# Optimization experiments

Hardware: AMD Instinct MI355X
Metric: run time of the kernel (lower is better)

Reference implementation:

```python
import jax, jax.numpy as jnp
import numpy as np

G, N, E, F, D = 4096, 64, 256, 64, 128
H1, H2 = 16, 2
EP = 32768
EPS = 1e-15
MAX_LOGSTD = 10.0


def setup_inputs() -> dict:
    key = jax.random.key(0)
    ks = jax.random.split(key, 16)
    def lin(k, i, o):
        return (jax.random.normal(k, (i, o), jnp.float32) / np.sqrt(i)).astype(jnp.float32)
    inp = {}
    inp["x"] = jax.random.normal(ks[0], (G, N, F), jnp.float32)
    inp["edge_index"] = jax.random.randint(ks[1], (G, 2, E), 0, N, dtype=jnp.int32)
    inp["edge_weight"] = jax.random.uniform(ks[2], (G, E), jnp.float32)
    inp["pos_edges"] = jax.random.randint(ks[3], (2, EP), 0, G, dtype=jnp.int32)
    inp["neg_edges"] = jax.random.randint(ks[4], (2, EP), 0, G, dtype=jnp.int32)
    inp["eps"] = jax.random.normal(ks[5], (G, D), jnp.float32)
    inp["W_gcn1"] = lin(ks[6], F, D); inp["b_gcn1"] = jnp.zeros((D,), jnp.float32)
    inp["W_fc1"] = lin(ks[7], D, H1); inp["b_fc1"] = jnp.zeros((H1,), jnp.float32)
    inp["W_fc2"] = lin(ks[8], H1, H2); inp["b_fc2"] = jnp.zeros((H2,), jnp.float32)
    inp["W_c1"] = lin(ks[9], D, 2 * D); inp["b_c1"] = jnp.zeros((2 * D,), jnp.float32)
    inp["W_mu"] = lin(ks[10], 2 * D, D); inp["b_mu"] = jnp.zeros((D,), jnp.float32)
    inp["W_ls"] = lin(ks[11], 2 * D, D); inp["b_ls"] = jnp.zeros((D,), jnp.float32)
    inp["emb"] = jax.random.normal(ks[12], (G, D), jnp.float32)
    inp["W_lin1"] = lin(ks[13], 2 * D, 2 * D); inp["b_lin1"] = jnp.zeros((2 * D,), jnp.float32)
    inp["W_lin2"] = lin(ks[14], 2 * D, 2 * D); inp["b_lin2"] = jnp.zeros((2 * D,), jnp.float32)
    return inp


def gcn_conv(x, src, dst, w, W, b, n):
    # PyG GCNConv: add self-loops (weight 1), sym-normalize, aggregate at target (col).
    xw = x @ W                                      # [n, out]
    deg = jnp.zeros((n,), xw.dtype).at[dst].add(w) + 1.0
    dinv = jax.lax.rsqrt(deg)
    norm = dinv[src] * w * dinv[dst]
    agg = jnp.zeros_like(xw).at[dst].add(xw[src] * norm[:, None])
    agg = agg + xw * (dinv * dinv)[:, None]         # self-loop term
    return agg + b


def sage_graph(x, ei, w, W_gcn1, b_gcn1, W_fc1, b_fc1, W_fc2, b_fc2):
    src, dst = ei[0], ei[1]
    h = gcn_conv(x, src, dst, w, W_gcn1, b_gcn1, N)          # [N, D]
    a1 = jnp.tanh(h @ W_fc1 + b_fc1)                         # [N, H1]
    S = jax.nn.softmax(a1 @ W_fc2 + b_fc2, axis=1)           # [N, 2]
    # get_laplacian(normalization='sym'): L = I - D^{-1/2} A D^{-1/2}, deg from row
    deg = jnp.zeros((N,), x.dtype).at[src].add(w)
    dinv = jnp.where(deg > 0, jax.lax.rsqrt(jnp.maximum(deg, 1e-30)), 0.0)
    lw = -dinv[src] * w * dinv[dst]
    L = jnp.zeros((N, N), x.dtype).at[src, dst].add(lw) + jnp.eye(N, dtype=x.dtype)
    new_adj = S.T @ (L @ S)                                  # [2, 2]
    norm_adj = new_adj / jnp.maximum(jnp.sum(jnp.abs(new_adj), axis=1, keepdims=True), 1e-12)
    diag = jnp.diagonal(norm_adj)
    pos_penalty = jnp.mean((diag - 1.0) ** 2)                # MSE vs ones(2)
    g_emb = jnp.mean(S.T @ h, axis=0)                        # [D]
    return g_emb, pos_penalty


def gcn_conv_unw(x, src, dst, W, b, n):
    return gcn_conv(x, src, dst, jnp.ones(src.shape, x.dtype), W, b, n)


def reference(x, edge_index, edge_weight, pos_edges, neg_edges, eps,
              W_gcn1, b_gcn1, W_fc1, b_fc1, W_fc2, b_fc2,
              W_c1, b_c1, W_mu, b_mu, W_ls, b_ls, emb,
              W_lin1, b_lin1, W_lin2, b_lin2):
    g_embs, pens = jax.vmap(sage_graph,
                            in_axes=(0, 0, 0, None, None, None, None, None, None))(
        x, edge_index, edge_weight, W_gcn1, b_gcn1, W_fc1, b_fc1, W_fc2, b_fc2)
    positive_penalty = jnp.mean(pens)
    # VGAE encode over graph-level graph (dropout in eval mode = identity)
    ps, pd = pos_edges[0], pos_edges[1]
    h = jax.nn.relu(gcn_conv_unw(g_embs, ps, pd, W_c1, b_c1, G))
    mu = gcn_conv_unw(h, ps, pd, W_mu, b_mu, G)
    logstd = jnp.minimum(gcn_conv_unw(h, ps, pd, W_ls, b_ls, G), MAX_LOGSTD)
    z = mu + eps * jnp.exp(logstd)                            # reparametrize
    zc = jnp.concatenate([emb, z], axis=-1)                   # [G, 2D]
    def pred(ei):
        fx = zc[ei[0]] @ W_lin1 + b_lin1
        fy = zc[ei[1]] @ W_lin2 + b_lin2
        return jax.nn.sigmoid(jnp.sum(fx * fy, axis=1))
    pos_pred = pred(pos_edges)
    neg_pred = pred(neg_edges)
    rec_loss = -jnp.mean(jnp.log(pos_pred + EPS)) - jnp.mean(jnp.log(1.0 - neg_pred + EPS))
    kl = -0.5 * jnp.mean(jnp.sum(1.0 + 2.0 * logstd - mu ** 2 - jnp.exp(2.0 * logstd), axis=1))
    pre_loss = rec_loss + kl / G
    return pre_loss, positive_penalty, pos_pred, neg_pred
```

## Files before the change

kernel.cpp:

```cpp
#include <hip/hip_runtime.h>
#include <hip/hip_bf16.h>
#include <math.h>

#define GG   4096
#define NNODE 64
#define EEDGE 256
#define FFEAT 64
#define DDIM 128
#define EP   32768

__global__ void k_prep(const float* __restrict__ Wg, const float* __restrict__ Wf1,
                       const float* __restrict__ bf1, const float* __restrict__ bg,
                       float* __restrict__ Wgf1, float* __restrict__ bcomb,
                       float* __restrict__ bg32) {
    int t = threadIdx.x;
    for (int o = t; o < 1024; o += 256) {
        int f = o >> 4, j = o & 15;
        float s = 0.f;
        for (int d = 0; d < 128; ++d) s += Wg[f * 128 + d] * Wf1[d * 16 + j];
        Wgf1[o] = s;
    }
    if (t < 16) {
        float s = bf1[t];
        for (int d = 0; d < 128; ++d) s += bg[d] * Wf1[d * 16 + t];
        bcomb[t] = s;
    }
    if (t >= 128) bg32[t - 128] = 32.0f * bg[t - 128];
}

__global__ __launch_bounds__(256) void k_pg(
    const float* __restrict__ x, const int* __restrict__ ei, const float* __restrict__ ew,
    const float* __restrict__ Wgf1, const float* __restrict__ bcomb,
    const float* __restrict__ Wf2, const float* __restrict__ bf2,
    float* __restrict__ Qh, float* __restrict__ pens)
{
    __shared__ __align__(16) float sm[8464];
    float* xs    = sm;
    float* Wgf1s = sm + 4352;
    float* a1s   = sm + 5376;
    int*   srcs  = (int*)(sm + 6400);
    int*   dsts  = (int*)(sm + 6656);
    float* lwx   = sm + 6912;
    int*   lsrc  = (int*)(sm + 7168);
    float* lnrm  = sm + 7424;
    int*   icnt  = (int*)(sm + 7680);
    int*   offs  = (int*)(sm + 7744);
    int*   curs  = (int*)(sm + 7808);
    float* degw  = sm + 7872;
    float* dinvs = sm + 7936;
    float* deg2s = sm + 8000;
    float* dinv2s= sm + 8064;
    float* Ss    = sm + 8128;
    float* Ssum  = sm + 8256;
    float* LSs   = sm + 8320;
    float* bcs   = sm + 8448;

    const int g = blockIdx.x;
    const int t = threadIdx.x;
    const float* xg = x + (size_t)g * 4096;

    {
        const int* eg = ei + (size_t)g * 512;
        srcs[t] = eg[t];
        dsts[t] = eg[256 + t];
        lwx[t]  = ew[(size_t)g * 256 + t];
        for (int i = t; i < 1024; i += 256) {
            int n = i >> 4, k = (i & 15) * 4;
            *(float4*)&xs[n * 68 + k] = *(const float4*)&xg[n * 64 + k];
        }
        for (int i = t; i < 1024; i += 256) Wgf1s[i] = Wgf1[i];
        if (t < 16) bcs[t] = bcomb[t];
        if (t < 64) { icnt[t] = 0; degw[t] = 1.0f; deg2s[t] = 0.0f; }
        if (t < 128) LSs[t] = 0.0f;
    }
    __syncthreads();

    {
        int dd = dsts[t], s = srcs[t];
        float w = lwx[t];
        atomicAdd(&icnt[dd], 1);
        atomicAdd(&degw[dd], w);
        atomicAdd(&deg2s[s], w);
    }
    __syncthreads();

    if (t < 64) {
        int v = icnt[t], own = v;
        for (int o = 1; o < 64; o <<= 1) { int u = __shfl_up(v, o); if (t >= o) v += u; }
        int excl = v - own;
        offs[t] = excl; curs[t] = excl;
        dinvs[t] = rsqrtf(degw[t]);
        float dg = deg2s[t];
        dinv2s[t] = dg > 0.0f ? rsqrtf(fmaxf(dg, 1e-30f)) : 0.0f;
    }
    __syncthreads();

    {
        int s = srcs[t], dd = dsts[t];
        float w = lwx[t];
        int pos = atomicAdd(&curs[dd], 1);
        lsrc[pos] = s;
        lnrm[pos] = dinvs[s] * w * dinvs[dd];
        lwx[t] = -dinv2s[s] * w * dinv2s[dd];
    }
    __syncthreads();

    {
        int n = t >> 2, base = (t & 3) * 16;
        float sc = dinvs[n] * dinvs[n];
        const float* xrow = &xs[n * 68 + base];
        float4 A0 = *(const float4*)&xrow[0];
        float4 A1 = *(const float4*)&xrow[4];
        float4 A2 = *(const float4*)&xrow[8];
        float4 A3 = *(const float4*)&xrow[12];
        A0.x *= sc; A0.y *= sc; A0.z *= sc; A0.w *= sc;
        A1.x *= sc; A1.y *= sc; A1.z *= sc; A1.w *= sc;
        A2.x *= sc; A2.y *= sc; A2.z *= sc; A2.w *= sc;
        A3.x *= sc; A3.y *= sc; A3.z *= sc; A3.w *= sc;
        int o = offs[n], c = icnt[n];
        for (int j = 0; j < c; ++j) {
            int s = lsrc[o + j];
            float nm = lnrm[o + j];
            const float* xr = &xs[s * 68 + base];
            float4 X0 = *(const float4*)&xr[0];
            float4 X1 = *(const float4*)&xr[4];
            float4 X2 = *(const float4*)&xr[8];
            float4 X3 = *(const float4*)&xr[12];
            A0.x += X0.x * nm; A0.y += X0.y * nm; A0.z += X0.z * nm; A0.w += X0.w * nm;
            A1.x += X1.x * nm; A1.y += X1.y * nm; A1.z += X1.z * nm; A1.w += X1.w * nm;
            A2.x += X2.x * nm; A2.y += X2.y * nm; A2.z += X2.z * nm; A2.w += X2.w * nm;
            A3.x += X3.x * nm; A3.y += X3.y * nm; A3.z += X3.z * nm; A3.w += X3.w * nm;
        }
        __syncthreads();
        float* xw = &xs[n * 68 + base];
        *(float4*)&xw[0]  = A0;
        *(float4*)&xw[4]  = A1;
        *(float4*)&xw[8]  = A2;
        *(float4*)&xw[12] = A3;
    }
    __syncthreads();

    {
        int n = t >> 2, j0 = (t & 3) * 4;
        float a0 = bcs[j0], a1v = bcs[j0 + 1], a2 = bcs[j0 + 2], a3 = bcs[j0 + 3];
#pragma unroll 4
        for (int k4 = 0; k4 < 16; ++k4) {
            float4 hv = *(const float4*)&xs[n * 68 + k4 * 4];
            float4 w0 = *(const float4*)&Wgf1s[(k4 * 4 + 0) * 16 + j0];
            float4 w1 = *(const float4*)&Wgf1s[(k4 * 4 + 1) * 16 + j0];
            float4 w2 = *(const float4*)&Wgf1s[(k4 * 4 + 2) * 16 + j0];
            float4 w3 = *(const float4*)&Wgf1s[(k4 * 4 + 3) * 16 + j0];
            a0  += hv.x * w0.x + hv.y * w1.x + hv.z * w2.x + hv.w * w3.x;
            a1v += hv.x * w0.y + hv.y * w1.y + hv.z * w2.y + hv.w * w3.y;
            a2  += hv.x * w0.z + hv.y * w1.z + hv.z * w2.z + hv.w * w3.z;
            a3  += hv.x * w0.w + hv.y * w1.w + hv.z * w2.w + hv.w * w3.w;
        }
        a1s[n * 16 + j0]     = tanhf(a0);
        a1s[n * 16 + j0 + 1] = tanhf(a1v);
        a1s[n * 16 + j0 + 2] = tanhf(a2);
        a1s[n * 16 + j0 + 3] = tanhf(a3);
    }
    __syncthreads();

    if (t < 128) {
        int n = t >> 1, kk = t & 1;
        float z = bf2[kk];
#pragma unroll
        for (int j = 0; j < 16; ++j) z += a1s[n * 16 + j] * Wf2[j * 2 + kk];
        Ss[n * 2 + kk] = z;
    }
    __syncthreads();

    if (t < 64) {
        float z0 = Ss[t * 2], z1 = Ss[t * 2 + 1];
        float m = fmaxf(z0, z1);
        float e0 = expf(z0 - m), e1 = expf(z1 - m);
        float inv = 1.0f / (e0 + e1);
        e0 *= inv; e1 *= inv;
        Ss[t * 2] = e0; Ss[t * 2 + 1] = e1;
        Ssum[t] = e0 + e1;
    }
    __syncthreads();

    for (int i = t; i < 512; i += 256) {
        int e = i >> 1, kk = i & 1;
        atomicAdd(&LSs[srcs[e] * 2 + kk], lwx[e] * Ss[dsts[e] * 2 + kk]);
    }
    __syncthreads();

    if (t < 64) {
        float s0 = Ss[t * 2], s1 = Ss[t * 2 + 1];
        float l0 = s0 + LSs[t * 2], l1 = s1 + LSs[t * 2 + 1];
        float p00 = s0 * l0, p01 = s0 * l1, p10 = s1 * l0, p11 = s1 * l1;
        for (int o = 32; o; o >>= 1) {
            p00 += __shfl_down(p00, o); p01 += __shfl_down(p01, o);
            p10 += __shfl_down(p10, o); p11 += __shfl_down(p11, o);
        }
        if (t == 0) {
            float r0 = fmaxf(fabsf(p00) + fabsf(p01), 1e-12f);
            float r1 = fmaxf(fabsf(p10) + fabsf(p11), 1e-12f);
            float d0 = p00 / r0 - 1.0f, d1 = p11 / r1 - 1.0f;
            pens[g] = 0.5f * (d0 * d0 + d1 * d1);
        }
    }
    {
        int k = t & 63, p = t >> 6;
        float qk = 0.f;
#pragma unroll 4
        for (int n = p * 16; n < p * 16 + 16; ++n)
            qk += Ssum[n] * xs[n * 68 + k];
        __syncthreads();
        a1s[p * 64 + k] = qk;
    }
    __syncthreads();
    if (t < 64)
        Qh[(size_t)g * 64 + t] = 0.5f * (a1s[t] + a1s[64 + t] + a1s[128 + t] + a1s[192 + t]);
}

__global__ void k_cnt(const int* __restrict__ pd, int* __restrict__ icnt) {
    int e = blockIdx.x * 256 + threadIdx.x;
    atomicAdd(&icnt[pd[e]], 1);
}

__global__ void k_scan(const int* __restrict__ icnt, int* __restrict__ offs,
                       int* __restrict__ curs, float* __restrict__ dinv) {
    __shared__ int wsum[4];
    int t = threadIdx.x;
    int base = t * 16;
    int l0,l1,l2,l3,l4,l5,l6,l7,l8,l9,l10,l11,l12,l13,l14,l15;
    l0=icnt[base+0]; l1=icnt[base+1]; l2=icnt[base+2]; l3=icnt[base+3];
    l4=icnt[base+4]; l5=icnt[base+5]; l6=icnt[base+6]; l7=icnt[base+7];
    l8=icnt[base+8]; l9=icnt[base+9]; l10=icnt[base+10]; l11=icnt[base+11];
    l12=icnt[base+12]; l13=icnt[base+13]; l14=icnt[base+14]; l15=icnt[base+15];
    int s = l0+l1+l2+l3+l4+l5+l6+l7+l8+l9+l10+l11+l12+l13+l14+l15;
    int lane = t & 63, w = t >> 6;
    int v = s;
    for (int o = 1; o < 64; o <<= 1) { int u = __shfl_up(v, o); if (lane >= o) v += u; }
    if (lane == 63) wsum[w] = v;
    __syncthreads();
    int woff = 0;
    for (int i = 0; i < 4; ++i) if (i < w) woff += wsum[i];
    int run = woff + v - s;
#define SC(L, I) offs[base+(I)] = run; curs[base+(I)] = run; \
    dinv[base+(I)] = rsqrtf((float)(L) + 1.0f); run += L;
    SC(l0,0) SC(l1,1) SC(l2,2) SC(l3,3) SC(l4,4) SC(l5,5) SC(l6,6) SC(l7,7)
    SC(l8,8) SC(l9,9) SC(l10,10) SC(l11,11) SC(l12,12) SC(l13,13) SC(l14,14) SC(l15,15)
#undef SC
}

__global__ void k_place(const int* __restrict__ pe, const float* __restrict__ dinv,
                        int* __restrict__ curs, int* __restrict__ csr_src,
                        float* __restrict__ csr_nrm) {
    int e = blockIdx.x * 256 + threadIdx.x;
    int s = pe[e], d = pe[EP + e];
    int pos = atomicAdd(&curs[d], 1);
    csr_src[pos] = s;
    csr_nrm[pos] = dinv[s] * dinv[d];
}

__global__ void k_gather128(const int* __restrict__ offs, const int* __restrict__ icnt,
                            const int* __restrict__ csr_src, const float* __restrict__ csr_nrm,
                            const float* __restrict__ dinv, const float* __restrict__ in,
                            float* __restrict__ out) {
    int g = blockIdx.x, d = threadIdx.x;
    float dv = dinv[g];
    float acc = in[(size_t)g * 128 + d] * dv * dv;
    int o = offs[g], c = icnt[g];
    for (int j = 0; j < c; ++j)
        acc += in[(size_t)csr_src[o + j] * 128 + d] * csr_nrm[o + j];
    out[(size_t)g * 128 + d] = acc;
}

__global__ void k_gather256(const int* __restrict__ offs, const int* __restrict__ icnt,
                            const int* __restrict__ csr_src, const float* __restrict__ csr_nrm,
                            const float* __restrict__ dinv, const float* __restrict__ in,
                            float* __restrict__ out) {
    int g = blockIdx.x, d = threadIdx.x;
    float dv = dinv[g];
    float acc = in[(size_t)g * 256 + d] * dv * dv;
    int o = offs[g], c = icnt[g];
    for (int j = 0; j < c; ++j)
        acc += in[(size_t)csr_src[o + j] * 256 + d] * csr_nrm[o + j];
    out[(size_t)g * 256 + d] = acc;
}

__global__ __launch_bounds__(256) void k_gemm(
    const float* __restrict__ A,
    const float* __restrict__ B0, const float* __restrict__ bias0, float* __restrict__ C0,
    const float* __restrict__ B1, const float* __restrict__ bias1, float* __restrict__ C1,
    int M, int K, int N, int dorelu)
{
    __shared__ __align__(16) float lds[2 * 4352];
    const float* B = B0; const float* bias = bias0; float* C = C0;
    int by = blockIdx.y;
    if (B1 != nullptr && by >= (int)(gridDim.y >> 1)) {
        B = B1; bias = bias1; C = C1; by -= (gridDim.y >> 1);
    }
    const int mb = blockIdx.x * 64, nbb = by * 64;
    const int t = threadIdx.x;
    const int tm4 = (t >> 4) * 4, tn4 = (t & 15) * 4;
    const int ma = t >> 2, ka = (t & 3) * 8;
    const int kb = t >> 3, nb8 = (t & 7) * 8;

    float4 pa0, pa1, pb0, pb1;
#define LOADT(K0) { \
    const float* Ap = &A[(size_t)(mb + ma) * K + (K0) + ka]; \
    pa0 = *(const float4*)Ap; pa1 = *(const float4*)(Ap + 4); \
    const float* Bp = &B[(size_t)((K0) + kb) * N + nbb + nb8]; \
    pb0 = *(const float4*)Bp; pb1 = *(const float4*)(Bp + 4); }
#define STORET(BUF) { \
    float* At_ = lds + (BUF) * 4352; \
    At_[(ka + 0) * 68 + ma] = pa0.x; At_[(ka + 1) * 68 + ma] = pa0.y; \
    At_[(ka + 2) * 68 + ma] = pa0.z; At_[(ka + 3) * 68 + ma] = pa0.w; \
    At_[(ka + 4) * 68 + ma] = pa1.x; At_[(ka + 5) * 68 + ma] = pa1.y; \
    At_[(ka + 6) * 68 + ma] = pa1.z; At_[(ka + 7) * 68 + ma] = pa1.w; \
    float* Bs_ = lds + (BUF) * 4352 + 2176; \
    *(float4*)&Bs_[kb * 68 + nb8] = pb0; *(float4*)&Bs_[kb * 68 + nb8 + 4] = pb1; }

    float4 ca0 = {0,0,0,0}, ca1 = {0,0,0,0}, ca2 = {0,0,0,0}, ca3 = {0,0,0,0};
    const int nk0 = K >> 5;
    LOADT(0)
    STORET(0)
    __syncthreads();
    for (int it = 0; it < nk0; ++it) {
        if (it + 1 < nk0) LOADT((it + 1) * 32)
        const float* At_ = lds + (it & 1) * 4352;
        const float* Bs_ = At_ + 2176;
#pragma unroll
        for (int k = 0; k < 32; ++k) {
            float4 av = *(const float4*)&At_[k * 68 + tm4];
            float4 bv = *(const float4*)&Bs_[k * 68 + tn4];
            ca0.x += av.x * bv.x; ca0.y += av.x * bv.y; ca0.z += av.x * bv.z; ca0.w += av.x * bv.w;
            ca1.x += av.y * bv.x; ca1.y += av.y * bv.y; ca1.z += av.y * bv.z; ca1.w += av.y * bv.w;
            ca2.x += av.z * bv.x; ca2.y += av.z * bv.y; ca2.z += av.z * bv.z; ca2.w += av.z * bv.w;
            ca3.x += av.w * bv.x; ca3.y += av.w * bv.y; ca3.z += av.w * bv.z; ca3.w += av.w * bv.w;
        }
        if (it + 1 < nk0) {
            STORET((it + 1) & 1)
            __syncthreads();
        }
    }
#undef LOADT
#undef STORET
    float4 bv4 = {0, 0, 0, 0};
    if (bias) bv4 = *(const float4*)&bias[nbb + tn4];
#define CST(I, CV) { \
    float4 v; v.x = CV.x + bv4.x; v.y = CV.y + bv4.y; v.z = CV.z + bv4.z; v.w = CV.w + bv4.w; \
    if (dorelu) { v.x = fmaxf(v.x, 0.f); v.y = fmaxf(v.y, 0.f); v.z = fmaxf(v.z, 0.f); v.w = fmaxf(v.w, 0.f); } \
    *(float4*)&C[(size_t)(mb + tm4 + (I)) * N + nbb + tn4] = v; }
    CST(0, ca0) CST(1, ca1) CST(2, ca2) CST(3, ca3)
#undef CST
}

__global__ void k_fin_z(const float* __restrict__ mu_arr, const float* __restrict__ ls_arr,
                        const float* __restrict__ eps, const float* __restrict__ emb,
                        float* __restrict__ zc, float* __restrict__ klp) {
    __shared__ float smw[2];
    int g = blockIdx.x, d = threadIdx.x;
    int idx = g * 128 + d;
    float mu = mu_arr[idx];
    float ls = fminf(ls_arr[idx], 10.0f);
    float z = mu + eps[idx] * expf(ls);
    zc[(size_t)g * 256 + d] = emb[idx];
    zc[(size_t)g * 256 + 128 + d] = z;
    float term = 1.0f + 2.0f * ls - mu * mu - expf(2.0f * ls);
    for (int o = 32; o; o >>= 1) term += __shfl_down(term, o);
    if ((d & 63) == 0) smw[d >> 6] = term;
    __syncthreads();
    if (d == 0) klp[g] = smw[0] + smw[1];
}

__global__ void k_pred(const float* __restrict__ A, const float* __restrict__ B,
                       const int* __restrict__ pos, const int* __restrict__ neg,
                       float* __restrict__ out, float* __restrict__ predp) {
    __shared__ float smw[16];
    int t = threadIdx.x, sub = t >> 4, l = t & 15;
    int eg = blockIdx.x * 16 + sub;
    int isneg = eg >= EP;
    int e = eg - (isneg ? EP : 0);
    const int* eix = isneg ? neg : pos;
    int s = eix[e], d = eix[EP + e];
    const float4* Ar = (const float4*)(A + (size_t)s * 256);
    const float4* Br = (const float4*)(B + (size_t)d * 256);
    float dot = 0.f;
#pragma unroll
    for (int q = 0; q < 4; ++q) {
        float4 av = Ar[l + 16 * q], bv = Br[l + 16 * q];
        dot += av.x * bv.x + av.y * bv.y + av.z * bv.z + av.w * bv.w;
    }
    for (int o = 8; o; o >>= 1) dot += __shfl_down(dot, o);
    if (l == 0) {
        float p = 1.0f / (1.0f + expf(-dot));
        float term;
        if (isneg) { out[2 + EP + e] = p; term = logf(1.0f - p + 1e-15f); }
        else       { out[2 + e] = p;      term = logf(p + 1e-15f); }
        smw[sub] = term;
    }
    __syncthreads();
    if (t == 0) {
        float s16 = 0.f;
#pragma unroll
        for (int i = 0; i < 16; ++i) s16 += smw[i];
        predp[blockIdx.x] = s16;
    }
}

__global__ void k_final(const float* __restrict__ pens, const float* __restrict__ klp,
                        const float* __restrict__ predp, float* __restrict__ out) {
    __shared__ float sm[16];
    int t = threadIdx.x;
    float s_pen = 0.f, s_kl = 0.f, s_pos = 0.f, s_neg = 0.f;
    for (int i = t; i < 4096; i += 256) { s_pen += pens[i]; s_kl += klp[i]; }
    for (int i = t; i < 2048; i += 256) { s_pos += predp[i]; s_neg += predp[2048 + i]; }
    for (int o = 32; o; o >>= 1) {
        s_pen += __shfl_down(s_pen, o); s_kl += __shfl_down(s_kl, o);
        s_pos += __shfl_down(s_pos, o); s_neg += __shfl_down(s_neg, o);
    }
    int w = t >> 6;
    if ((t & 63) == 0) { sm[w] = s_pen; sm[4 + w] = s_kl; sm[8 + w] = s_pos; sm[12 + w] = s_neg; }
    __syncthreads();
    if (t == 0) {
        float pen = sm[0] + sm[1] + sm[2] + sm[3];
        float kls = sm[4] + sm[5] + sm[6] + sm[7];
        float pos = sm[8] + sm[9] + sm[10] + sm[11];
        float neg = sm[12] + sm[13] + sm[14] + sm[15];
        float rec = -(pos / 32768.0f) - (neg / 32768.0f);
        out[0] = rec - 0.5f * kls / (4096.0f * 4096.0f);
        out[1] = pen * (1.0f / 4096.0f);
    }
}

extern "C" void kernel_launch(void* const* d_in, const int* in_sizes, int n_in,
                              void* d_out, int out_size, void* d_ws, size_t ws_size,
                              hipStream_t stream) {
    const float* x   = (const float*)d_in[0];
    const int*   ei  = (const int*)d_in[1];
    const float* ew  = (const float*)d_in[2];
    const int*   pos = (const int*)d_in[3];
    const int*   neg = (const int*)d_in[4];
    const float* eps = (const float*)d_in[5];
    const float* Wg  = (const float*)d_in[6];
    const float* bg  = (const float*)d_in[7];
    const float* Wf1 = (const float*)d_in[8];
    const float* bf1 = (const float*)d_in[9];
    const float* Wf2 = (const float*)d_in[10];
    const float* bf2 = (const float*)d_in[11];
    const float* Wc1 = (const float*)d_in[12];
    const float* bc1 = (const float*)d_in[13];
    const float* Wmu = (const float*)d_in[14];
    const float* bmu = (const float*)d_in[15];
    const float* Wls = (const float*)d_in[16];
    const float* bls = (const float*)d_in[17];
    const float* emb = (const float*)d_in[18];
    const float* Wl1 = (const float*)d_in[19];
    const float* bl1 = (const float*)d_in[20];
    const float* Wl2 = (const float*)d_in[21];
    const float* bl2 = (const float*)d_in[22];
    float* out = (float*)d_out;
    float* ws  = (float*)d_ws;

    float* g_embs  = ws + 0;
    float* dinv    = ws + 524288;
    int*   icnt_g  = (int*)(ws + 528384);
    int*   off_g   = (int*)(ws + 532480);
    int*   cur_g   = (int*)(ws + 536576);
    int*   csr_src = (int*)(ws + 540672);
    float* csr_nrm = ws + 573440;
    float* Qh      = ws + 606208;
    float* ga      = ws + 868352;
    float* h       = ws + 1392640;
    float* ha      = ws + 2441216;
    float* mu_arr  = ws + 3489792;
    float* ls_arr  = ws + 4014080;
    float* zc      = ws + 4538368;
    float* Abuf    = ws + 5586944;
    float* Bbuf    = ws + 6635520;
    float* pens    = ws + 7684096;
    float* klp     = ws + 7688192;
    float* predp   = ws + 7692288;
    float* Wgf1    = ws + 7708672;
    float* bcomb   = ws + 7709696;
    float* bg32    = ws + 7709712;

    hipMemsetAsync(icnt_g, 0, 4096u * 4, stream);

    k_prep<<<1, 256, 0, stream>>>(Wg, Wf1, bf1, bg, Wgf1, bcomb, bg32);
    k_pg<<<GG, 256, 0, stream>>>(x, ei, ew, Wgf1, bcomb, Wf2, bf2, Qh, pens);
    k_gemm<<<dim3(64, 2), 256, 0, stream>>>(Qh, Wg, bg32, g_embs,
                                            nullptr, nullptr, nullptr, GG, 64, 128, 0);

    k_cnt<<<EP / 256, 256, 0, stream>>>(pos + EP, icnt_g);
    k_scan<<<1, 256, 0, stream>>>(icnt_g, off_g, cur_g, dinv);
    k_place<<<EP / 256, 256, 0, stream>>>(pos, dinv, cur_g, csr_src, csr_nrm);

    k_gather128<<<GG, 128, 0, stream>>>(off_g, icnt_g, csr_src, csr_nrm, dinv, g_embs, ga);
    k_gemm<<<dim3(64, 4), 256, 0, stream>>>(ga, Wc1, bc1, h,
                                            nullptr, nullptr, nullptr, GG, 128, 256, 1);

    k_gather256<<<GG, 256, 0, stream>>>(off_g, icnt_g, csr_src, csr_nrm, dinv, h, ha);
    k_gemm<<<dim3(64, 4), 256, 0, stream>>>(ha, Wmu, bmu, mu_arr,
                                            Wls, bls, ls_arr, GG, 256, 128, 0);
    k_fin_z<<<GG, 128, 0, stream>>>(mu_arr, ls_arr, eps, emb, zc, klp);

    k_gemm<<<dim3(64, 8), 256, 0, stream>>>(zc, Wl1, bl1, Abuf,
                                            Wl2, bl2, Bbuf, GG, 256, 256, 0);

    k_pred<<<(2 * EP) / 16, 256, 0, stream>>>(Abuf, Bbuf, pos, neg, out, predp);
    k_final<<<1, 256, 0, stream>>>(pens, klp, predp, out);
}
```

Before: 320.5 us.

## Project node features to hidden width before aggregation in per-graph kernel

Adds a separate kernel that multiplies all node features by the fused Wgf1 weight (64->16) before graph aggregation. The per-graph kernel then aggregates 16-wide rows instead of 64-wide ones, which shrinks its shared memory and aggregation work. The Q readout is reformulated as a weighted sum of the raw x rows, with weights built by scattering edge norms times the softmax sums. This avoids keeping the aggregated 64-wide features, but x is read twice from global memory and a 4096x64x16 intermediate is written and read back. The intermediate reuses the h workspace region.

```diff
diff --git a/kernel.cpp b/kernel.cpp
--- a/kernel.cpp
+++ b/kernel.cpp
@@ -28,60 +28,97 @@
     if (t >= 128) bg32[t - 128] = 32.0f * bg[t - 128];
 }
 
+__global__ __launch_bounds__(256) void k_xw(
+    const float* __restrict__ x, const float* __restrict__ Wgf1,
+    float* __restrict__ xwg)
+{
+    __shared__ __align__(16) float Ws[1024];
+    const int t = threadIdx.x;
+    for (int i = t; i < 1024; i += 256) Ws[i] = Wgf1[i];
+    __syncthreads();
+    const size_t r0 = (size_t)blockIdx.x * 512 + t;
+    const float* x0 = x + r0 * 64;
+    const float* x1 = x + (r0 + 256) * 64;
+    float4 z = {0, 0, 0, 0};
+    float4 c00 = z, c01 = z, c02 = z, c03 = z;
+    float4 c10 = z, c11 = z, c12 = z, c13 = z;
+#pragma unroll
+    for (int k4 = 0; k4 < 16; ++k4) {
+        float4 a0 = *(const float4*)&x0[k4 * 4];
+        float4 a1 = *(const float4*)&x1[k4 * 4];
+#define STEP(KK, E) { \
+        const float* wr = &Ws[(k4 * 4 + (KK)) * 16]; \
+        float4 w0 = *(const float4*)wr,       w1 = *(const float4*)(wr + 4); \
+        float4 w2 = *(const float4*)(wr + 8), w3 = *(const float4*)(wr + 12); \
+        c00.x += a0.E * w0.x; c00.y += a0.E * w0.y; c00.z += a0.E * w0.z; c00.w += a0.E * w0.w; \
+        c01.x += a0.E * w1.x; c01.y += a0.E * w1.y; c01.z += a0.E * w1.z; c01.w += a0.E * w1.w; \
+        c02.x += a0.E * w2.x; c02.y += a0.E * w2.y; c02.z += a0.E * w2.z; c02.w += a0.E * w2.w; \
+        c03.x += a0.E * w3.x; c03.y += a0.E * w3.y; c03.z += a0.E * w3.z; c03.w += a0.E * w3.w; \
+        c10.x += a1.E * w0.x; c10.y += a1.E * w0.y; c10.z += a1.E * w0.z; c10.w += a1.E * w0.w; \
+        c11.x += a1.E * w1.x; c11.y += a1.E * w1.y; c11.z += a1.E * w1.z; c11.w += a1.E * w1.w; \
+        c12.x += a1.E * w2.x; c12.y += a1.E * w2.y; c12.z += a1.E * w2.z; c12.w += a1.E * w2.w; \
+        c13.x += a1.E * w3.x; c13.y += a1.E * w3.y; c13.z += a1.E * w3.z; c13.w += a1.E * w3.w; }
+        STEP(0, x) STEP(1, y) STEP(2, z) STEP(3, w)
+#undef STEP
+    }
+    float* o0 = &xwg[r0 * 16];
+    *(float4*)&o0[0] = c00; *(float4*)&o0[4] = c01;
+    *(float4*)&o0[8] = c02; *(float4*)&o0[12] = c03;
+    float* o1 = &xwg[(r0 + 256) * 16];
+    *(float4*)&o1[0] = c10; *(float4*)&o1[4] = c11;
+    *(float4*)&o1[8] = c12; *(float4*)&o1[12] = c13;
+}
+
 __global__ __launch_bounds__(256) void k_pg(
-    const float* __restrict__ x, const int* __restrict__ ei, const float* __restrict__ ew,
-    const float* __restrict__ Wgf1, const float* __restrict__ bcomb,
+    const float* __restrict__ x, const float* __restrict__ xwg,
+    const int* __restrict__ ei, const float* __restrict__ ew,
+    const float* __restrict__ bcomb,
     const float* __restrict__ Wf2, const float* __restrict__ bf2,
     float* __restrict__ Qh, float* __restrict__ pens)
 {
-    __shared__ __align__(16) float sm[8464];
-    float* xs    = sm;
-    float* Wgf1s = sm + 4352;
-    float* a1s   = sm + 5376;
-    int*   srcs  = (int*)(sm + 6400);
-    int*   dsts  = (int*)(sm + 6656);
-    float* lwx   = sm + 6912;
-    int*   lsrc  = (int*)(sm + 7168);
-    float* lnrm  = sm + 7424;
-    int*   icnt  = (int*)(sm + 7680);
-    int*   offs  = (int*)(sm + 7744);
-    int*   curs  = (int*)(sm + 7808);
-    float* degw  = sm + 7872;
-    float* dinvs = sm + 7936;
-    float* deg2s = sm + 8000;
-    float* dinv2s= sm + 8064;
-    float* Ss    = sm + 8128;
-    float* Ssum  = sm + 8256;
-    float* LSs   = sm + 8320;
-    float* bcs   = sm + 8448;
+    __shared__ __align__(16) float sm[4688];
+    float* xws   = sm;
+    float* a1s   = sm + 1280;
+    int*   srcs  = (int*)(sm + 2304);
+    int*   dsts  = (int*)(sm + 2560);
+    float* lwx   = sm + 2816;
+    int*   lsrc  = (int*)(sm + 3072);
+    float* lnrm  = sm + 3328;
+    float* enrm  = sm + 3584;
+    int*   icnt  = (int*)(sm + 3840);
+    int*   offs  = (int*)(sm + 3904);
+    int*   curs  = (int*)(sm + 3968);
+    float* degw  = sm + 4032;
+    float* dinvs = sm + 4096;
+    float* deg2s = sm + 4160;
+    float* dinv2s= sm + 4224;
+    float* wv    = sm + 4288;
+    float* Ss    = sm + 4352;
+    float* Ssum  = sm + 4480;
+    float* LSs   = sm + 4544;
+    float* bcs   = sm + 4672;
 
     const int g = blockIdx.x;
     const int t = threadIdx.x;
-    const float* xg = x + (size_t)g * 4096;
-
+
+    const int* eg = ei + (size_t)g * 512;
+    const int sR = eg[t];
+    const int dR = eg[256 + t];
+    const float wR = ew[(size_t)g * 256 + t];
     {
-        const int* eg = ei + (size_t)g * 512;
-        srcs[t] = eg[t];
-        dsts[t] = eg[256 + t];
-        lwx[t]  = ew[(size_t)g * 256 + t];
-        for (int i = t; i < 1024; i += 256) {
-            int n = i >> 4, k = (i & 15) * 4;
-            *(float4*)&xs[n * 68 + k] = *(const float4*)&xg[n * 64 + k];
-        }
-        for (int i = t; i < 1024; i += 256) Wgf1s[i] = Wgf1[i];
-        if (t < 16) bcs[t] = bcomb[t];
-        if (t < 64) { icnt[t] = 0; degw[t] = 1.0f; deg2s[t] = 0.0f; }
-        if (t < 128) LSs[t] = 0.0f;
-    }
-    __syncthreads();
-
-    {
-        int dd = dsts[t], s = srcs[t];
-        float w = lwx[t];
-        atomicAdd(&icnt[dd], 1);
-        atomicAdd(&degw[dd], w);
-        atomicAdd(&deg2s[s], w);
-    }
+        int n = t >> 2, j4 = (t & 3) * 4;
+        float4 v = *(const float4*)&xwg[(size_t)g * 1024 + n * 16 + j4];
+        *(float4*)&xws[n * 20 + j4] = v;
+    }
+    srcs[t] = sR; dsts[t] = dR;
+    if (t < 16) bcs[t] = bcomb[t];
+    if (t < 64) { icnt[t] = 0; degw[t] = 1.0f; deg2s[t] = 0.0f; }
+    if (t < 128) LSs[t] = 0.0f;
+    __syncthreads();
+
+    atomicAdd(&icnt[dR], 1);
+    atomicAdd(&degw[dR], wR);
+    atomicAdd(&deg2s[sR], wR);
     __syncthreads();
 
     if (t < 64) {
@@ -96,69 +133,32 @@
     __syncthreads();
 
     {
-        int s = srcs[t], dd = dsts[t];
-        float w = lwx[t];
-        int pos = atomicAdd(&curs[dd], 1);
-        lsrc[pos] = s;
-        lnrm[pos] = dinvs[s] * w * dinvs[dd];
-        lwx[t] = -dinv2s[s] * w * dinv2s[dd];
+        int pos = atomicAdd(&curs[dR], 1);
+        float nm = dinvs[sR] * wR * dinvs[dR];
+        lsrc[pos] = sR;
+        lnrm[pos] = nm;
+        enrm[t] = nm;
+        lwx[t] = -dinv2s[sR] * wR * dinv2s[dR];
     }
     __syncthreads();
 
     {
-        int n = t >> 2, base = (t & 3) * 16;
-        float sc = dinvs[n] * dinvs[n];
-        const float* xrow = &xs[n * 68 + base];
-        float4 A0 = *(const float4*)&xrow[0];
-        float4 A1 = *(const float4*)&xrow[4];
-        float4 A2 = *(const float4*)&xrow[8];
-        float4 A3 = *(const float4*)&xrow[12];
-        A0.x *= sc; A0.y *= sc; A0.z *= sc; A0.w *= sc;
-        A1.x *= sc; A1.y *= sc; A1.z *= sc; A1.w *= sc;
-        A2.x *= sc; A2.y *= sc; A2.z *= sc; A2.w *= sc;
-        A3.x *= sc; A3.y *= sc; A3.z *= sc; A3.w *= sc;
+        int n = t >> 2, j4 = (t & 3) * 4;
+        float dv = dinvs[n], sc = dv * dv;
+        float4 A = *(const float4*)&xws[n * 20 + j4];
+        A.x *= sc; A.y *= sc; A.z *= sc; A.w *= sc;
         int o = offs[n], c = icnt[n];
         for (int j = 0; j < c; ++j) {
             int s = lsrc[o + j];
             float nm = lnrm[o + j];
-            const float* xr = &xs[s * 68 + base];
-            float4 X0 = *(const float4*)&xr[0];
-            float4 X1 = *(const float4*)&xr[4];
-            float4 X2 = *(const float4*)&xr[8];
-            float4 X3 = *(const float4*)&xr[12];
-            A0.x += X0.x * nm; A0.y += X0.y * nm; A0.z += X0.z * nm; A0.w += X0.w * nm;
-            A1.x += X1.x * nm; A1.y += X1.y * nm; A1.z += X1.z * nm; A1.w += X1.w * nm;
-            A2.x += X2.x * nm; A2.y += X2.y * nm; A2.z += X2.z * nm; A2.w += X2.w * nm;
-            A3.x += X3.x * nm; A3.y += X3.y * nm; A3.z += X3.z * nm; A3.w += X3.w * nm;
+            float4 X = *(const float4*)&xws[s * 20 + j4];
+            A.x += X.x * nm; A.y += X.y * nm; A.z += X.z * nm; A.w += X.w * nm;
         }
-        __syncthreads();
-        float* xw = &xs[n * 68 + base];
-        *(float4*)&xw[0]  = A0;
-        *(float4*)&xw[4]  = A1;
-        *(float4*)&xw[8]  = A2;
-        *(float4*)&xw[12] = A3;
-    }
-    __syncthreads();
-
-    {
-        int n = t >> 2, j0 = (t & 3) * 4;
-        float a0 = bcs[j0], a1v = bcs[j0 + 1], a2 = bcs[j0 + 2], a3 = bcs[j0 + 3];
-#pragma unroll 4
-        for (int k4 = 0; k4 < 16; ++k4) {
-            float4 hv = *(const float4*)&xs[n * 68 + k4 * 4];
-            float4 w0 = *(const float4*)&Wgf1s[(k4 * 4 + 0) * 16 + j0];
-            float4 w1 = *(const float4*)&Wgf1s[(k4 * 4 + 1) * 16 + j0];
-            float4 w2 = *(const float4*)&Wgf1s[(k4 * 4 + 2) * 16 + j0];
-            float4 w3 = *(const float4*)&Wgf1s[(k4 * 4 + 3) * 16 + j0];
-            a0  += hv.x * w0.x + hv.y * w1.x + hv.z * w2.x + hv.w * w3.x;
-            a1v += hv.x * w0.y + hv.y * w1.y + hv.z * w2.y + hv.w * w3.y;
-            a2  += hv.x * w0.z + hv.y * w1.z + hv.z * w2.z + hv.w * w3.z;
-            a3  += hv.x * w0.w + hv.y * w1.w + hv.z * w2.w + hv.w * w3.w;
-        }
-        a1s[n * 16 + j0]     = tanhf(a0);
-        a1s[n * 16 + j0 + 1] = tanhf(a1v);
-        a1s[n * 16 + j0 + 2] = tanhf(a2);
-        a1s[n * 16 + j0 + 3] = tanhf(a3);
+        float4 bb = *(const float4*)&bcs[j4];
+        a1s[n * 16 + j4 + 0] = tanhf(A.x + bb.x);
+        a1s[n * 16 + j4 + 1] = tanhf(A.y + bb.y);
+        a1s[n * 16 + j4 + 2] = tanhf(A.z + bb.z);
+        a1s[n * 16 + j4 + 3] = tanhf(A.w + bb.w);
     }
     __syncthreads();
 
@@ -178,7 +178,9 @@
         float inv = 1.0f / (e0 + e1);
         e0 *= inv; e1 *= inv;
         Ss[t * 2] = e0; Ss[t * 2 + 1] = e1;
-        Ssum[t] = e0 + e1;
+        float su = e0 + e1;
+        Ssum[t] = su;
+        wv[t] = dinvs[t] * dinvs[t] * su;
     }
     __syncthreads();
 
@@ -186,6 +188,7 @@
         int e = i >> 1, kk = i & 1;
         atomicAdd(&LSs[srcs[e] * 2 + kk], lwx[e] * Ss[dsts[e] * 2 + kk]);
     }
+    atomicAdd(&wv[sR], enrm[t] * Ssum[dR]);
     __syncthreads();
 
     if (t < 64) {
@@ -205,11 +208,11 @@
     }
     {
         int k = t & 63, p = t >> 6;
+        const float* xg = x + (size_t)g * 4096 + (p * 16) * 64 + k;
         float qk = 0.f;
-#pragma unroll 4
-        for (int n = p * 16; n < p * 16 + 16; ++n)
-            qk += Ssum[n] * xs[n * 68 + k];
-        __syncthreads();
+#pragma unroll
+        for (int n = 0; n < 16; ++n)
+            qk += wv[p * 16 + n] * xg[n * 64];
         a1s[p * 64 + k] = qk;
     }
     __syncthreads();
@@ -469,6 +472,7 @@
     float* Qh      = ws + 606208;
     float* ga      = ws + 868352;
     float* h       = ws + 1392640;
+    float* xwg     = ws + 1392640;
     float* ha      = ws + 2441216;
     float* mu_arr  = ws + 3489792;
     float* ls_arr  = ws + 4014080;
@@ -485,7 +489,8 @@
     hipMemsetAsync(icnt_g, 0, 4096u * 4, stream);
 
     k_prep<<<1, 256, 0, stream>>>(Wg, Wf1, bf1, bg, Wgf1, bcomb, bg32);
-    k_pg<<<GG, 256, 0, stream>>>(x, ei, ew, Wgf1, bcomb, Wf2, bf2, Qh, pens);
+    k_xw<<<512, 256, 0, stream>>>(x, Wgf1, xwg);
+    k_pg<<<GG, 256, 0, stream>>>(x, xwg, ei, ew, bcomb, Wf2, bf2, Qh, pens);
     k_gemm<<<dim3(64, 2), 256, 0, stream>>>(Qh, Wg, bg32, g_embs,
                                             nullptr, nullptr, nullptr, GG, 64, 128, 0);
 
```

Measured after the change: 332.6 us. 3.8% more time.
